# Optimization experiments

Measured on AMD Instinct MI355X. Metric: run time of the kernel, lower is better.

The kernel has to match this reference:

```python
import jax, jax.numpy as jnp
import numpy as np

B, P, L = 16, 32, 512
M = 32
L_EVAL = 2048


def setup_inputs() -> dict:
    key = jax.random.key(0)
    k1, k2, k3, k4, k5, k6 = jax.random.split(key, 6)
    # Sorted, positive event times per (B, P) path in [0, 1)
    event_times = jnp.sort(jax.random.uniform(k1, (B, P, L), dtype=jnp.float32), axis=-1)
    # Positive Hawkes parameters (as if post-Softplus)
    mu = jax.random.uniform(k2, (B, M, P, L), dtype=jnp.float32, minval=0.05, maxval=1.0)
    alpha = jax.random.uniform(k3, (B, M, P, L), dtype=jnp.float32, minval=0.05, maxval=2.0)
    beta = jax.random.uniform(k4, (B, M, P, L), dtype=jnp.float32, minval=0.1, maxval=5.0)
    # Positive per-batch normalisation constants
    norm_constants = jax.random.uniform(k5, (B,), dtype=jnp.float32, minval=0.5, maxval=1.5)
    # Query times on the ORIGINAL time axis (normalized_times=False path)
    query_times = jax.random.uniform(k6, (B, P, L_EVAL), dtype=jnp.float32, minval=0.0, maxval=1.5)
    return {
        "query_times": query_times,
        "event_times": event_times,
        "mu": mu,
        "alpha": alpha,
        "beta": beta,
        "norm_constants": norm_constants,
    }


def reference(query_times, event_times, mu, alpha, beta, norm_constants):
    # query_times: [B,P,Le]; event_times: [B,P,L]; mu/alpha/beta: [B,M,P,L]; norm_constants: [B]
    b, p, le = query_times.shape
    m = mu.shape[1]
    nc = norm_constants.reshape(b, 1, 1)
    q_norm = query_times / nc  # map to normalised axis (normalized_times=False)

    # searchsorted per (B,P) row: index of last event strictly before t
    ss = jax.vmap(jax.vmap(lambda a, v: jnp.searchsorted(a, v, side="left")))
    last_idx = ss(event_times, q_norm).astype(jnp.int32) - 1      # [B,P,Le]
    last_idx_cl = jnp.maximum(last_idx, 0)                         # clamp(min=0)

    # Gather parameters of the latest preceding event along L
    gidx = jnp.broadcast_to(last_idx_cl[:, None, :, :], (b, m, p, le))
    mu_last = jnp.take_along_axis(mu, gidx, axis=3)                # [B,M,P,Le]
    alpha_last = jnp.take_along_axis(alpha, gidx, axis=3)
    beta_last = jnp.take_along_axis(beta, gidx, axis=3)

    t_last = jnp.take_along_axis(event_times, last_idx_cl, axis=2)  # [B,P,Le]
    t_last = jnp.where(last_idx == -1, jnp.zeros_like(t_last), t_last)

    delta_t = (q_norm - t_last)[:, None, :, :]                      # [B,1,P,Le]
    intensity = mu_last + (alpha_last - mu_last) * jnp.exp(-beta_last * delta_t)
    # back to original scale
    intensity = intensity / norm_constants.reshape(b, 1, 1, 1)
    return intensity
```

## Files before the change

kernel.cpp:

```cpp
#include <hip/hip_runtime.h>

#define B_  16
#define P_  32
#define L_  512
#define M_  32
#define LE_ 2048

#define MSPLIT 8
#define MC     (M_ / MSPLIT)


__device__ __forceinline__ void gload_lds16(const float* g, float* l) {
    __builtin_amdgcn_global_load_lds(
        (const __attribute__((address_space(1))) void*)g,
        (__attribute__((address_space(3))) void*)l, 16, 0, 0);
}

__global__ __launch_bounds__(512) void hawkes_intensity_kernel(
    const float* __restrict__ q,
    const float* __restrict__ ev,
    const float* __restrict__ mu,
    const float* __restrict__ alpha,
    const float* __restrict__ beta,
    const float* __restrict__ nc,
    float* __restrict__ out)
{
    __shared__ float sev[L_];
    __shared__ float smu[MSPLIT][L_];
    __shared__ float sal[MSPLIT][L_];
    __shared__ float sbe[MSPLIT][L_];

    const int bid = blockIdx.x;
    const int mc  = bid & (MC - 1);
    const int row = bid >> 2;
    const int b   = row / P_;
    const int p   = row % P_;
    const int m0  = mc * MSPLIT;
    const int tid = threadIdx.x;

    const float* evrow = ev + (size_t)row * L_;
    const float e0 = (tid < L_) ? evrow[tid] : 0.0f;
    const float4 qv = *(const float4*)(q + (size_t)row * LE_ + 4 * tid);

    sev[tid] = e0;

    const size_t pbase   = (((size_t)b * M_ + m0) * P_ + p) * L_;
    const size_t mstride = (size_t)P_ * L_;
    #pragma unroll
    for (int i = 0; i < 2; ++i) {
        const int fidx = tid + 512 * i;
        const int ml   = fidx >> 7;
        const int l4   = (fidx & 127) << 2;
        const int fb   = (tid & ~63) + 512 * i;
        const int l4b  = (fb & 127) << 2;
        const size_t g = pbase + (size_t)ml * mstride + l4;
        gload_lds16(mu    + g, &smu[ml][l4b]);
        gload_lds16(alpha + g, &sal[ml][l4b]);
        gload_lds16(beta  + g, &sbe[ml][l4b]);
    }

    asm volatile("s_waitcnt lgkmcnt(0)" ::: "memory");
    __builtin_amdgcn_s_barrier();
    __builtin_amdgcn_sched_barrier(0);

    const float ncv    = nc[b];
    const float inv_nc = (float)(1.0 / (double)ncv);

    int   idx[4];
    float dt[4];
    #pragma unroll
    for (int i = 0; i < 4; ++i) {
        const float qn = ((const float*)&qv)[i] * inv_nc;
        int pos = 0;
        #pragma unroll
        for (int half = 256; half >= 1; half >>= 1) {
            const int cand = pos + half;
            pos = (sev[cand - 1] < qn) ? cand : pos;
        }
        pos += (sev[pos] < qn) ? 1 : 0;
        const int last = pos - 1;
        idx[i] = (last < 0) ? 0 : last;
        const float tl = (last < 0) ? 0.0f : sev[idx[i]];
        dt[i] = qn - tl;
    }

    __syncthreads();

    const int le0 = 4 * tid;
    const size_t obase = (((size_t)b * M_ + m0) * P_ + p) * LE_ + le0;
    #pragma unroll
    for (int m = 0; m < MSPLIT; ++m) {
        float4 o;
        #pragma unroll
        for (int i = 0; i < 4; ++i) {
            const int   ix  = idx[i];
            const float mul = smu[m][ix];
            const float al  = sal[m][ix];
            const float be  = sbe[m][ix];
            ((float*)&o)[i] = (mul + (al - mul) * __expf(-be * dt[i])) * inv_nc;
        }
        *(float4*)(out + obase + (size_t)m * ((size_t)P_ * LE_)) = o;
    }
}

extern "C" void kernel_launch(void* const* d_in, const int* in_sizes, int n_in,
                              void* d_out, int out_size, void* d_ws, size_t ws_size,
                              hipStream_t stream) {
    const float* q     = (const float*)d_in[0];
    const float* ev    = (const float*)d_in[1];
    const float* mu    = (const float*)d_in[2];
    const float* alpha = (const float*)d_in[3];
    const float* beta  = (const float*)d_in[4];
    const float* nc    = (const float*)d_in[5];
    float* out = (float*)d_out;

    dim3 grid(B_ * P_ * MC);
    dim3 block(512);
    hipLaunchKernelGGL(hawkes_intensity_kernel, grid, block, 0, stream,
                       q, ev, mu, alpha, beta, nc, out);
}
```

Baseline: 43.36 us.

## Pack mu/alpha/beta as bf16 into shared memory and load after search

Replaces the async global-to-LDS loads of mu, alpha and beta with register loads issued after the binary search. Each value is rounded to bf16 and the three are packed into one uint2 per LDS entry, so the gather needs one 8-byte LDS read instead of three scalar reads, and shared memory per block shrinks. Launch bounds now request higher occupancy. The bf16 rounding loses precision on the parameters and may exceed tolerance, and the loads no longer overlap with the search.

```diff
diff --git a/kernel.cpp b/kernel.cpp
--- a/kernel.cpp
+++ b/kernel.cpp
@@ -10,13 +10,12 @@
 #define MC     (M_ / MSPLIT)
 
 
-__device__ __forceinline__ void gload_lds16(const float* g, float* l) {
-    __builtin_amdgcn_global_load_lds(
-        (const __attribute__((address_space(1))) void*)g,
-        (__attribute__((address_space(3))) void*)l, 16, 0, 0);
+__device__ __forceinline__ unsigned bf16_rne(float x) {
+    unsigned u = __float_as_uint(x);
+    return (u + 0x7FFFu + ((u >> 16) & 1u)) >> 16;
 }
 
-__global__ __launch_bounds__(512) void hawkes_intensity_kernel(
+__global__ __launch_bounds__(512, 8) void hawkes_intensity_kernel(
     const float* __restrict__ q,
     const float* __restrict__ ev,
     const float* __restrict__ mu,
@@ -26,9 +25,7 @@
     float* __restrict__ out)
 {
     __shared__ float sev[L_];
-    __shared__ float smu[MSPLIT][L_];
-    __shared__ float sal[MSPLIT][L_];
-    __shared__ float sbe[MSPLIT][L_];
+    __shared__ uint2 spack[MSPLIT][L_];
 
     const int bid = blockIdx.x;
     const int mc  = bid & (MC - 1);
@@ -38,33 +35,15 @@
     const int m0  = mc * MSPLIT;
     const int tid = threadIdx.x;
 
-    const float* evrow = ev + (size_t)row * L_;
-    const float e0 = (tid < L_) ? evrow[tid] : 0.0f;
+    const float  e0 = ev[(size_t)row * L_ + tid];
     const float4 qv = *(const float4*)(q + (size_t)row * LE_ + 4 * tid);
-
     sev[tid] = e0;
-
-    const size_t pbase   = (((size_t)b * M_ + m0) * P_ + p) * L_;
-    const size_t mstride = (size_t)P_ * L_;
-    #pragma unroll
-    for (int i = 0; i < 2; ++i) {
-        const int fidx = tid + 512 * i;
-        const int ml   = fidx >> 7;
-        const int l4   = (fidx & 127) << 2;
-        const int fb   = (tid & ~63) + 512 * i;
-        const int l4b  = (fb & 127) << 2;
-        const size_t g = pbase + (size_t)ml * mstride + l4;
-        gload_lds16(mu    + g, &smu[ml][l4b]);
-        gload_lds16(alpha + g, &sal[ml][l4b]);
-        gload_lds16(beta  + g, &sbe[ml][l4b]);
-    }
 
     asm volatile("s_waitcnt lgkmcnt(0)" ::: "memory");
     __builtin_amdgcn_s_barrier();
     __builtin_amdgcn_sched_barrier(0);
 
-    const float ncv    = nc[b];
-    const float inv_nc = (float)(1.0 / (double)ncv);
+    const float inv_nc = (float)(1.0 / (double)nc[b]);
 
     int   idx[4];
     float dt[4];
@@ -84,19 +63,37 @@
         dt[i] = qn - tl;
     }
 
+    const size_t pbase   = (((size_t)b * M_ + m0) * P_ + p) * L_;
+    const size_t mstride = (size_t)P_ * L_;
+    #pragma unroll
+    for (int i = 0; i < 2; ++i) {
+        const int fidx = tid + 512 * i;
+        const int ml   = fidx >> 7;
+        const int l4   = (fidx & 127) << 2;
+        const size_t g = pbase + (size_t)ml * mstride + l4;
+        const float4 fm = *(const float4*)(mu    + g);
+        const float4 fa = *(const float4*)(alpha + g);
+        const float4 fb = *(const float4*)(beta  + g);
+        #pragma unroll
+        for (int k = 0; k < 4; ++k) {
+            const unsigned bm = bf16_rne(((const float*)&fm)[k]);
+            const unsigned ba = bf16_rne(((const float*)&fa)[k]);
+            const unsigned bb = bf16_rne(((const float*)&fb)[k]);
+            spack[ml][l4 + k] = make_uint2(bm | (ba << 16), bb);
+        }
+    }
     __syncthreads();
 
-    const int le0 = 4 * tid;
-    const size_t obase = (((size_t)b * M_ + m0) * P_ + p) * LE_ + le0;
+    const size_t obase = (((size_t)b * M_ + m0) * P_ + p) * LE_ + 4 * tid;
     #pragma unroll
     for (int m = 0; m < MSPLIT; ++m) {
         float4 o;
         #pragma unroll
         for (int i = 0; i < 4; ++i) {
-            const int   ix  = idx[i];
-            const float mul = smu[m][ix];
-            const float al  = sal[m][ix];
-            const float be  = sbe[m][ix];
+            const uint2 e   = spack[m][idx[i]];
+            const float mul = __uint_as_float(e.x << 16);
+            const float al  = __uint_as_float(e.x & 0xFFFF0000u);
+            const float be  = __uint_as_float(e.y << 16);
             ((float*)&o)[i] = (mul + (al - mul) * __expf(-be * dt[i])) * inv_nc;
         }
         *(float4*)(out + obase + (size_t)m * ((size_t)P_ * LE_)) = o;
```

New measurement: 43.89 us. About the same (+1.2%).
